# Optimization experiments

Hardware: AMD Instinct MI355X
Metric: run time of the kernel (lower is better)

The kernel has to match this reference:

```python
import jax, jax.numpy as jnp
import numpy as np
from math import pi

N = 256        # in_features == out_features
BATCH = 131072


def givens_orthogonal(angles, n):
    """Build an n x n orthogonal matrix as the ordered product of Givens
    rotations G(i, j, theta_k) over pairs i < j in lexicographic order.
    Each rotation mixes rows i and j; applied sequentially via lax.scan."""
    ii, jj = np.triu_indices(n, 1)  # static pair order, len = n*(n-1)//2
    ii = jnp.asarray(ii, dtype=jnp.int32)
    jj = jnp.asarray(jj, dtype=jnp.int32)

    def body(M, t):
        i, j, th = t
        c, s = jnp.cos(th), jnp.sin(th)
        ri, rj = M[i], M[j]
        M = M.at[i].set(c * ri - s * rj)
        M = M.at[j].set(s * ri + c * rj)
        return M, None

    M0 = jnp.eye(n, dtype=angles.dtype)
    M, _ = jax.lax.scan(body, M0, (ii, jj, angles))
    return M


def setup_inputs() -> dict:
    key = jax.random.key(0)
    k1, k2, k3 = jax.random.split(key, 3)
    n_ang = N * (N - 1) // 2  # 32640
    return {
        "x": jax.random.normal(k1, (BATCH, N), dtype=jnp.float32),
        "Uweight": jax.random.uniform(k2, (n_ang,), minval=-pi / 2, maxval=pi / 2, dtype=jnp.float32),
        "Vweight": jax.random.uniform(k3, (n_ang,), minval=-pi / 2, maxval=pi / 2, dtype=jnp.float32),
        "Sweight": jnp.ones((N,), dtype=jnp.float32),
        "bias": jnp.zeros((N,), dtype=jnp.float32),
    }


def reference(x, Uweight, Vweight, Sweight, bias):
    # W = V @ diag(S) @ U^T  (SVD-parametrized weight, out x in)
    # y = x @ W^T + b = ((x @ U) * S) @ V^T + b   (square case in == out)
    U = givens_orthogonal(Uweight, N)  # (in, in) orthogonal
    V = givens_orthogonal(Vweight, N)  # (out, out) orthogonal
    return ((x @ U) * Sweight) @ V.T + bias
```

## Files before the change

kernel.cpp:

```cpp
#include <hip/hip_runtime.h>
#include <hip/hip_bf16.h>
#include <math.h>

#define NN 256
#define NPAIR 32640
#define NSEG 32
#define MAT (NN*NN)

#define CS_U 0
#define CS_V (2*NPAIR)
#define MATS0 131072
#define MATS1 (MATS0 + 64*MAT)
#define WBT_OFF (MATS1 + 32*MAT)

static __device__ const int BD[NSEG+1] =
    {0,4,8,12,16,20,24,28,32,37,42,47,52,57,62,67,73,79,85,91,97,
     104,111,118,126,134,143,153,164,177,192,213,255};
#define CSL_CAP 1120

typedef __attribute__((ext_vector_type(8))) short short8;
typedef __attribute__((ext_vector_type(4))) float f32x4;

__device__ __forceinline__ short f2bf(float f) {
    __hip_bfloat16 h = __float2bfloat16(f);
    return *reinterpret_cast<short*>(&h);
}

__global__ __launch_bounds__(256) void k_sincos(const float* __restrict__ au,
                                                const float* __restrict__ av,
                                                float* __restrict__ ws) {
    int id = blockIdx.x * 256 + threadIdx.x;
    if (id < NPAIR) {
        float s, c;
        sincosf(au[id], &s, &c);
        ws[CS_U + 2*id]     = c;
        ws[CS_U + 2*id + 1] = s;
    } else if (id < 2*NPAIR) {
        int k = id - NPAIR;
        float s, c;
        sincosf(av[k], &s, &c);
        ws[CS_V + 2*k]     = c;
        ws[CS_V + 2*k + 1] = s;
    }
}

__global__ __launch_bounds__(64) void k_build(const float* __restrict__ ws,
                                              float* __restrict__ mats) {
    int b = blockIdx.x;
    int matid = b >> 7;
    int seg   = (b >> 2) & 31;
    int chunk = b & 3;
    int t = threadIdx.x;
    int c0 = chunk * 64;
    int i0 = BD[seg], i1 = BD[seg+1];
    float* outp = mats + (matid * NSEG + seg) * MAT;

    if (c0 + 64 <= i0) {
        for (int id = t; id < 4096; id += 64) {
            int row = id >> 4, c4 = (id & 15) * 4;
            float4 v = {0.f,0.f,0.f,0.f};
            int d = row - (c0 + c4);
            if (d >= 0 && d < 4) ((float*)&v)[d] = 1.0f;
            *(float4*)(outp + row*NN + c0 + c4) = v;
        }
        return;
    }

    __shared__ float M[NN * 64];
    __shared__ float2 csl[CSL_CAP];

    int kbase = 255*i0 - (i0*(i0-1))/2;
    int kend  = 255*i1 - (i1*(i1-1))/2;
    int nrot  = kend - kbase;
    const float* cs = ws + (matid ? CS_V : CS_U) + 2*kbase;
    for (int idx = t; idx < nrot; idx += 64)
        csl[idx] = *(const float2*)(cs + 2*idx);

    int MR = NN - i0;
    for (int rr = 0; rr < MR; ++rr)
        M[rr*64 + t] = (i0 + rr == c0 + t) ? 1.0f : 0.0f;
    __syncthreads();

    for (int i = i0; i < i1; ++i) {
        int jstart = (i + 1 > c0) ? (i + 1) : c0;
        int kl = 255*i - (i*(i-1))/2 + (jstart - i - 1) - kbase;
        float ri = M[(i - i0)*64 + t];
        int j = jstart;
        int ng = (NN - jstart) >> 3;

        float2 cb[8]; float rj[8];
        if (ng > 0) {
#pragma unroll
            for (int u = 0; u < 8; ++u) cb[u] = csl[kl + u];
#pragma unroll
            for (int u = 0; u < 8; ++u) rj[u] = M[(j - i0 + u)*64 + t];
        }
        for (int g = 0; g < ng; ++g) {
            float2 cn[8]; float rn[8];
            if (g + 1 < ng) {
#pragma unroll
                for (int u = 0; u < 8; ++u) cn[u] = csl[kl + 8 + u];
#pragma unroll
                for (int u = 0; u < 8; ++u) rn[u] = M[(j + 8 - i0 + u)*64 + t];
            }
#pragma unroll
            for (int u = 0; u < 8; ++u) {
                float wv = cb[u].y*ri + cb[u].x*rj[u];
                ri       = cb[u].x*ri - cb[u].y*rj[u];
                M[(j - i0 + u)*64 + t] = wv;
            }
#pragma unroll
            for (int u = 0; u < 8; ++u) { cb[u] = cn[u]; rj[u] = rn[u]; }
            j += 8; kl += 8;
        }
        int rem = NN - j;
        if (rem > 0) {
            float2 cc[7]; float r7[7];
#pragma unroll
            for (int u = 0; u < 7; ++u)
                if (u < rem) { cc[u] = csl[kl + u];
                               r7[u] = M[(j - i0 + u)*64 + t]; }
#pragma unroll
            for (int u = 0; u < 7; ++u)
                if (u < rem) {
                    float wv = cc[u].y*ri + cc[u].x*r7[u];
                    ri       = cc[u].x*ri - cc[u].y*r7[u];
                    M[(j - i0 + u)*64 + t] = wv;
                }
        }
        M[(i - i0)*64 + t] = ri;
    }
    __syncthreads();

    for (int id = t; id < 4096; id += 64) {
        int row = id >> 4, c4 = (id & 15) * 4;
        float4 v;
        if (row < i0) {
            v = make_float4(0.f,0.f,0.f,0.f);
            int d = row - (c0 + c4);
            if (d >= 0 && d < 4) ((float*)&v)[d] = 1.0f;
        } else {
            v = *(const float4*)&M[(row - i0)*64 + c4];
        }
        *(float4*)(outp + row*NN + c0 + c4) = v;
    }
}

__global__ __launch_bounds__(256) void k_fold(const float* __restrict__ in,
                                              float* __restrict__ out,
                                              int nOut, int lg, int span) {
    int b = blockIdx.x;
    int np2 = 2 * nOut;
    int m    = b & (np2 - 1);
    int tile = b >> lg;
    int side = (m >= nOut) ? 1 : 0;
    int q = m - side * nOut;
    const float* A = in + (side*np2 + 2*q + 1) * MAT;
    const float* B = in + (side*np2 + 2*q) * MAT;
    float* C = out + m * MAT;
    int i0A = BD[q * span + (span >> 1)];
    int r0 = (tile >> 2) * 64, c0 = (tile & 3) * 64;
    int t = threadIdx.x;

    if (r0 + 64 <= i0A) {
#pragma unroll
        for (int u = 0; u < 4; ++u) {
            int id = u*256 + t;
            int rr = id >> 4, cc = (id & 15) * 4;
            *(float4*)(C + (r0+rr)*NN + c0 + cc) =
                *(const float4*)(B + (r0+rr)*NN + c0 + cc);
        }
        return;
    }

    int kstart = ((r0 < i0A) ? r0 : i0A) & ~31;
    int nt = (NN - kstart) >> 5;

    __shared__ float Ast[2][32][68];
    __shared__ float Bs [2][32][68];
    int tx = t & 15, ty = t >> 4;
    int arow = t >> 3, ak4 = t & 7;
    int bkr = t >> 4, bc4 = t & 15;

    float acc[4][4] = {};
    f32x4 pa0, pa1, pb0, pb1;
    {
        int kt = kstart;
        pa0 = *(const f32x4*)(A + (r0 + arow     )*NN + kt + ak4*4);
        pa1 = *(const f32x4*)(A + (r0 + arow + 32)*NN + kt + ak4*4);
        pb0 = *(const f32x4*)(B + (kt + bkr      )*NN + c0 + bc4*4);
        pb1 = *(const f32x4*)(B + (kt + bkr + 16 )*NN + c0 + bc4*4);
    }
    for (int it = 0; it < nt; ++it) {
        int cur = it & 1;
#pragma unroll
        for (int jj = 0; jj < 4; ++jj) {
            Ast[cur][ak4*4 + jj][arow]      = pa0[jj];
            Ast[cur][ak4*4 + jj][arow + 32] = pa1[jj];
        }
        *(f32x4*)&Bs[cur][bkr     ][bc4*4] = pb0;
        *(f32x4*)&Bs[cur][bkr + 16][bc4*4] = pb1;
        if (it + 1 < nt) {
            int k2 = kstart + (it+1)*32;
            pa0 = *(const f32x4*)(A + (r0 + arow     )*NN + k2 + ak4*4);
            pa1 = *(const f32x4*)(A + (r0 + arow + 32)*NN + k2 + ak4*4);
            pb0 = *(const f32x4*)(B + (k2 + bkr      )*NN + c0 + bc4*4);
            pb1 = *(const f32x4*)(B + (k2 + bkr + 16 )*NN + c0 + bc4*4);
        }
        __syncthreads();
#pragma unroll 8
        for (int kk = 0; kk < 32; ++kk) {
            f32x4 a4 = *(const f32x4*)&Ast[cur][kk][ty*4];
            f32x4 b4 = *(const f32x4*)&Bs [cur][kk][tx*4];
#pragma unroll
            for (int rr = 0; rr < 4; ++rr)
#pragma unroll
                for (int cc = 0; cc < 4; ++cc)
                    acc[rr][cc] = fmaf(a4[rr], b4[cc], acc[rr][cc]);
        }
    }
#pragma unroll
    for (int rr = 0; rr < 4; ++rr) {
        float4 o = {acc[rr][0], acc[rr][1], acc[rr][2], acc[rr][3]};
        *(float4*)(C + (r0 + ty*4 + rr)*NN + c0 + tx*4) = o;
    }
}

__global__ __launch_bounds__(256) void k_wmatT(const float* __restrict__ U,
                                               const float* __restrict__ V,
                                               const float* __restrict__ S,
                                               unsigned short* __restrict__ Wbt) {
    int b = blockIdx.x;
    int n0 = (b >> 4) * 16, i0 = (b & 15) * 16;
    int t = threadIdx.x, ti = t & 15, tn = t >> 4;
    __shared__ float Us[16][260];
    __shared__ float Vs[16][260];
    {
        int rr = t >> 4, cc = (t & 15) * 16;
#pragma unroll
        for (int q = 0; q < 4; ++q) {
            float4 u = *(const float4*)(U + (i0+rr)*NN + cc + q*4);
            float4 s = *(const float4*)(S + cc + q*4);
            u.x *= s.x; u.y *= s.y; u.z *= s.z; u.w *= s.w;
            *(float4*)&Us[rr][cc+q*4] = u;
            *(float4*)&Vs[rr][cc+q*4] = *(const float4*)(V + (n0+rr)*NN + cc + q*4);
        }
    }
    __syncthreads();
    float acc = 0.f;
#pragma unroll 8
    for (int k4 = 0; k4 < 64; ++k4) {
        float4 uu = *(const float4*)&Us[ti][k4*4];
        float4 vv = *(const float4*)&Vs[tn][k4*4];
        acc += uu.x*vv.x + uu.y*vv.y + uu.z*vv.z + uu.w*vv.w;
    }
    Wbt[(n0+tn)*NN + (i0+ti)] = (unsigned short)f2bf(acc);
}

__global__ __launch_bounds__(512, 4) void k_mm(const float* __restrict__ x,
                                               const unsigned short* __restrict__ Wbt,
                                               const float* __restrict__ bias,
                                               float* __restrict__ out) {
    int t = threadIdx.x;
    int w = t >> 6, l = t & 63, l15 = l & 15, lg = l >> 4;
    int n0 = w * 32;

    __shared__ unsigned short Xs[2][16 * 264];

    short8 bfrag[2][8];
#pragma unroll
    for (int nt = 0; nt < 2; ++nt) {
        const unsigned short* wrow = Wbt + (n0 + nt*16 + l15) * NN + lg * 8;
#pragma unroll
        for (int ks = 0; ks < 8; ++ks)
            bfrag[nt][ks] = *(const short8*)(wrow + ks * 32);
    }
    float b0 = bias[n0 + l15];
    float b1 = bias[n0 + 16 + l15];

    int row  = t >> 5;
    int col8 = (t & 31) * 8;

    int tile = blockIdx.x;
    const float* src = x + (long)tile * 4096 + row * NN + col8;
    float4 f0 = *(const float4*)(src);
    float4 f1 = *(const float4*)(src + 4);

    for (int it = 0; it < 8; ++it, tile += 1024) {
        int cur = it & 1;
        short8 h;
        h[0]=f2bf(f0.x); h[1]=f2bf(f0.y); h[2]=f2bf(f0.z); h[3]=f2bf(f0.w);
        h[4]=f2bf(f1.x); h[5]=f2bf(f1.y); h[6]=f2bf(f1.z); h[7]=f2bf(f1.w);
        *(short8*)&Xs[cur][row * 264 + col8] = h;
        if (it < 7) {
            const float* s2 = x + (long)(tile + 1024) * 4096 + row * NN + col8;
            f0 = *(const float4*)(s2);
            f1 = *(const float4*)(s2 + 4);
        }
        __syncthreads();

        f32x4 acc0 = {0.f,0.f,0.f,0.f}, acc1 = {0.f,0.f,0.f,0.f};
        const unsigned short* xs = &Xs[cur][l15 * 264 + lg * 8];
#pragma unroll
        for (int ks = 0; ks < 8; ++ks) {
            short8 af = *(const short8*)(xs + ks * 32);
            acc0 = __builtin_amdgcn_mfma_f32_16x16x32_bf16(af, bfrag[0][ks], acc0, 0, 0, 0);
            acc1 = __builtin_amdgcn_mfma_f32_16x16x32_bf16(af, bfrag[1][ks], acc1, 0, 0, 0);
        }
        float* op = out + ((long)tile * 16 + lg * 4) * NN + n0 + l15;
#pragma unroll
        for (int r = 0; r < 4; ++r) {
            op[r * NN]      = acc0[r] + b0;
            op[r * NN + 16] = acc1[r] + b1;
        }
    }
}

extern "C" void kernel_launch(void* const* d_in, const int* in_sizes, int n_in,
                              void* d_out, int out_size, void* d_ws, size_t ws_size,
                              hipStream_t stream) {
    const float* x    = (const float*)d_in[0];
    const float* Uw   = (const float*)d_in[1];
    const float* Vw   = (const float*)d_in[2];
    const float* Sw   = (const float*)d_in[3];
    const float* bias = (const float*)d_in[4];
    float* out = (float*)d_out;
    float* ws  = (float*)d_ws;

    k_sincos<<<255, 256, 0, stream>>>(Uw, Vw, ws);
    k_build<<<256, 64, 0, stream>>>(ws, ws + MATS0);
    k_fold<<<16*32, 256, 0, stream>>>(ws + MATS0, ws + MATS1, 16, 5, 2);
    k_fold<<<16*16, 256, 0, stream>>>(ws + MATS1, ws + MATS0,  8, 4, 4);
    k_fold<<<16* 8, 256, 0, stream>>>(ws + MATS0, ws + MATS1,  4, 3, 8);
    k_fold<<<16* 4, 256, 0, stream>>>(ws + MATS1, ws + MATS0,  2, 2, 16);
    k_fold<<<16* 2, 256, 0, stream>>>(ws + MATS0, ws + MATS1,  1, 1, 32);
    k_wmatT<<<256, 256, 0, stream>>>(ws + MATS1, ws + MATS1 + MAT, Sw,
                                     (unsigned short*)(ws + WBT_OFF));
    k_mm<<<1024, 512, 0, stream>>>(x, (unsigned short*)(ws + WBT_OFF), bias, out);
}
```

Before: 194.6 us.

## Fuse sincos into build kernel and restructure GEMM to one-shot 32-row tiles

Removes the separate sincos kernel and computes cos/sin of the angles directly inside k_build when filling shared memory, saving one launch and a workspace round-trip. The GEMM kernel changes from 1024 blocks looping over 8 double-buffered 16-row tiles to 4096 blocks that each load 32 rows once. The X tile in LDS now uses a fragment-ordered layout so each lane reads its MFMA operand contiguously. The trade-off is that the B fragments from Wbt are reloaded by four times as many blocks, and load latency is no longer hidden by in-block prefetch.

```diff
diff --git a/kernel.cpp b/kernel.cpp
--- a/kernel.cpp
+++ b/kernel.cpp
@@ -7,9 +7,7 @@
 #define NSEG 32
 #define MAT (NN*NN)
 
-#define CS_U 0
-#define CS_V (2*NPAIR)
-#define MATS0 131072
+#define MATS0 0
 #define MATS1 (MATS0 + 64*MAT)
 #define WBT_OFF (MATS1 + 32*MAT)
 
@@ -26,25 +24,8 @@
     return *reinterpret_cast<short*>(&h);
 }
 
-__global__ __launch_bounds__(256) void k_sincos(const float* __restrict__ au,
-                                                const float* __restrict__ av,
-                                                float* __restrict__ ws) {
-    int id = blockIdx.x * 256 + threadIdx.x;
-    if (id < NPAIR) {
-        float s, c;
-        sincosf(au[id], &s, &c);
-        ws[CS_U + 2*id]     = c;
-        ws[CS_U + 2*id + 1] = s;
-    } else if (id < 2*NPAIR) {
-        int k = id - NPAIR;
-        float s, c;
-        sincosf(av[k], &s, &c);
-        ws[CS_V + 2*k]     = c;
-        ws[CS_V + 2*k + 1] = s;
-    }
-}
-
-__global__ __launch_bounds__(64) void k_build(const float* __restrict__ ws,
+__global__ __launch_bounds__(64) void k_build(const float* __restrict__ au,
+                                              const float* __restrict__ av,
                                               float* __restrict__ mats) {
     int b = blockIdx.x;
     int matid = b >> 7;
@@ -72,9 +53,13 @@
     int kbase = 255*i0 - (i0*(i0-1))/2;
     int kend  = 255*i1 - (i1*(i1-1))/2;
     int nrot  = kend - kbase;
-    const float* cs = ws + (matid ? CS_V : CS_U) + 2*kbase;
-    for (int idx = t; idx < nrot; idx += 64)
-        csl[idx] = *(const float2*)(cs + 2*idx);
+    const float* ang = (matid ? av : au) + kbase;
+    for (int idx = t; idx < nrot; idx += 64) {
+        float s, c;
+        sincosf(ang[idx], &s, &c);
+        float2 v = {c, s};
+        csl[idx] = v;
+    }
 
     int MR = NN - i0;
     for (int rr = 0; rr < MR; ++rr)
@@ -265,7 +250,7 @@
     int w = t >> 6, l = t & 63, l15 = l & 15, lg = l >> 4;
     int n0 = w * 32;
 
-    __shared__ unsigned short Xs[2][16 * 264];
+    __shared__ unsigned short Xs[16 * 512];
 
     short8 bfrag[2][8];
 #pragma unroll
@@ -278,40 +263,39 @@
     float b0 = bias[n0 + l15];
     float b1 = bias[n0 + 16 + l15];
 
-    int row  = t >> 5;
-    int col8 = (t & 31) * 8;
-
-    int tile = blockIdx.x;
-    const float* src = x + (long)tile * 4096 + row * NN + col8;
-    float4 f0 = *(const float4*)(src);
-    float4 f1 = *(const float4*)(src + 4);
-
-    for (int it = 0; it < 8; ++it, tile += 1024) {
-        int cur = it & 1;
-        short8 h;
-        h[0]=f2bf(f0.x); h[1]=f2bf(f0.y); h[2]=f2bf(f0.z); h[3]=f2bf(f0.w);
-        h[4]=f2bf(f1.x); h[5]=f2bf(f1.y); h[6]=f2bf(f1.z); h[7]=f2bf(f1.w);
-        *(short8*)&Xs[cur][row * 264 + col8] = h;
-        if (it < 7) {
-            const float* s2 = x + (long)(tile + 1024) * 4096 + row * NN + col8;
-            f0 = *(const float4*)(s2);
-            f1 = *(const float4*)(s2 + 4);
-        }
-        __syncthreads();
-
+    long row0 = (long)blockIdx.x * 32;
+    int r = t & 15, m = t >> 4;
+    int ksb = m >> 2;
+    int lidx = r + 16 * (m & 3);
+    const float* s0 = x + (row0 + r) * NN + 8*m;
+    const float* s1 = s0 + 16 * NN;
+    float4 a0 = *(const float4*)(s0);
+    float4 a1 = *(const float4*)(s0 + 4);
+    float4 c0 = *(const float4*)(s1);
+    float4 c1 = *(const float4*)(s1 + 4);
+    short8 h0, h1;
+    h0[0]=f2bf(a0.x); h0[1]=f2bf(a0.y); h0[2]=f2bf(a0.z); h0[3]=f2bf(a0.w);
+    h0[4]=f2bf(a1.x); h0[5]=f2bf(a1.y); h0[6]=f2bf(a1.z); h0[7]=f2bf(a1.w);
+    h1[0]=f2bf(c0.x); h1[1]=f2bf(c0.y); h1[2]=f2bf(c0.z); h1[3]=f2bf(c0.w);
+    h1[4]=f2bf(c1.x); h1[5]=f2bf(c1.y); h1[6]=f2bf(c1.z); h1[7]=f2bf(c1.w);
+    *(short8*)&Xs[(0*8 + ksb)*512 + lidx*8] = h0;
+    *(short8*)&Xs[(1*8 + ksb)*512 + lidx*8] = h1;
+    __syncthreads();
+
+#pragma unroll
+    for (int tt = 0; tt < 2; ++tt) {
         f32x4 acc0 = {0.f,0.f,0.f,0.f}, acc1 = {0.f,0.f,0.f,0.f};
-        const unsigned short* xs = &Xs[cur][l15 * 264 + lg * 8];
 #pragma unroll
         for (int ks = 0; ks < 8; ++ks) {
-            short8 af = *(const short8*)(xs + ks * 32);
+            short8 af = *(const short8*)&Xs[(tt*8 + ks)*512 + l*8];
             acc0 = __builtin_amdgcn_mfma_f32_16x16x32_bf16(af, bfrag[0][ks], acc0, 0, 0, 0);
             acc1 = __builtin_amdgcn_mfma_f32_16x16x32_bf16(af, bfrag[1][ks], acc1, 0, 0, 0);
         }
-        float* op = out + ((long)tile * 16 + lg * 4) * NN + n0 + l15;
-#pragma unroll
-        for (int r = 0; r < 4; ++r) {
-            op[r * NN]      = acc0[r] + b0;
-            op[r * NN + 16] = acc1[r] + b1;
+        float* op = out + (row0 + tt*16 + lg*4) * NN + n0 + l15;
+#pragma unroll
+        for (int rr = 0; rr < 4; ++rr) {
+            op[rr * NN]      = acc0[rr] + b0;
+            op[rr * NN + 16] = acc1[rr] + b1;
         }
     }
 }
@@ -327,8 +311,7 @@
     float* out = (float*)d_out;
     float* ws  = (float*)d_ws;
 
-    k_sincos<<<255, 256, 0, stream>>>(Uw, Vw, ws);
-    k_build<<<256, 64, 0, stream>>>(ws, ws + MATS0);
+    k_build<<<256, 64, 0, stream>>>(Uw, Vw, ws + MATS0);
     k_fold<<<16*32, 256, 0, stream>>>(ws + MATS0, ws + MATS1, 16, 5, 2);
     k_fold<<<16*16, 256, 0, stream>>>(ws + MATS1, ws + MATS0,  8, 4, 4);
     k_fold<<<16* 8, 256, 0, stream>>>(ws + MATS0, ws + MATS1,  4, 3, 8);
@@ -336,5 +319,5 @@
     k_fold<<<16* 2, 256, 0, stream>>>(ws + MATS0, ws + MATS1,  1, 1, 32);
     k_wmatT<<<256, 256, 0, stream>>>(ws + MATS1, ws + MATS1 + MAT, Sw,
                                      (unsigned short*)(ws + WBT_OFF));
-    k_mm<<<1024, 512, 0, stream>>>(x, (unsigned short*)(ws + WBT_OFF), bias, out);
-}
+    k_mm<<<4096, 512, 0, stream>>>(x, (unsigned short*)(ws + WBT_OFF), bias, out);
+}
```

Measured after the change: 227.6 us. 17.0% more time.
